# Performance work log

Measured on AMD Instinct MI355X. Metric: run time of the kernel, lower is better.

The kernel has to match this reference:

```python
import jax, jax.numpy as jnp
import numpy as np

N_NODES = 50000
N_EDGES = 800000
HIDDEN = 128
NUM_GDL = 2


def setup_inputs() -> dict:
    key = jax.random.key(0)
    k0, k1, k2, k3, k4 = jax.random.split(key, 5)
    x = jax.random.normal(k0, (N_NODES, HIDDEN), dtype=jnp.float32)
    row = jax.random.randint(k1, (N_EDGES,), 0, N_NODES, dtype=jnp.int32)
    # ensure every node appears at least once as a target so degree >= 1
    col_tail = jax.random.randint(k2, (N_EDGES - N_NODES,), 0, N_NODES, dtype=jnp.int32)
    col = jnp.concatenate([jnp.arange(N_NODES, dtype=jnp.int32), col_tail])
    edge_index = jnp.stack([row, col], axis=0)  # [2, E]
    W1s = jax.random.normal(k3, (NUM_GDL, HIDDEN, HIDDEN), dtype=jnp.float32) / np.sqrt(HIDDEN).astype(np.float32)
    W2s = jax.random.normal(k4, (NUM_GDL, HIDDEN, 2 * HIDDEN), dtype=jnp.float32) / np.sqrt(2 * HIDDEN).astype(np.float32)
    biases = jnp.zeros((NUM_GDL, HIDDEN), dtype=jnp.float32)  # reset_parameters zeroes bias
    return {"x": x, "edge_index": edge_index, "W1s": W1s, "W2s": W2s, "biases": biases}


def reference(x, edge_index, W1s, W2s, biases):
    # eval mode: dropout is identity
    row, col = edge_index[0], edge_index[1]  # row = source j, col = target i
    n, d = x.shape
    deg = jax.ops.segment_sum(jnp.ones(row.shape[0], x.dtype), col, num_segments=n)
    norm = (1.0 / deg)[row]  # per-edge norm, indexed by row as in torch source
    for k in range(W1s.shape[0]):
        W1, W2, b = W1s[k], W2s[k], biases[k]
        # lin2(cat[x_i, x_j]) = x_i @ W2[:, :d].T + x_j @ W2[:, d:].T
        # precompute both node-level projections, then gather per edge (cheaper than per-edge GEMM)
        proj_i = x @ W2[:, :d].T  # [n, d]
        proj_j = x @ W2[:, d:].T  # [n, d]
        msg = norm[:, None] * (proj_i[col] + proj_j[row])  # [E, d]
        agg = jax.ops.segment_sum(msg, col, num_segments=n)  # scatter-add into targets
        out = x @ W1.T - agg + b
        x = jax.nn.gelu(out, approximate=False)  # torch nn.GELU default = exact erf
    return x
```

## Files before the change

### kernel.cpp

```cpp
#include <hip/hip_runtime.h>

#define N_NODES 50000
#define N_EDGES 800000
#define D 128
#define NBUCKET 196
#define CAP 8192
#define EPT 16
#define SCAT_BLOCKS 196
#define WCONV_BLOCKS 96
#define GEMM_TILES 391

typedef unsigned short ushort_t;
typedef __bf16 bf16x8 __attribute__((ext_vector_type(8)));
typedef float f32x4 __attribute__((ext_vector_type(4)));
typedef float f32x2 __attribute__((ext_vector_type(2)));

__device__ __forceinline__ ushort_t f2bf(float f) {
    unsigned u = __builtin_bit_cast(unsigned, f);
    u += 0x7FFFu + ((u >> 16) & 1u);
    return (ushort_t)(u >> 16);
}
__device__ __forceinline__ float bf2f(unsigned h16) {
    return __builtin_bit_cast(float, h16 << 16);
}

__global__ __launch_bounds__(256) void k_pre(const int* __restrict__ row, const int* __restrict__ col,
                                             int* __restrict__ bucket_cursor, unsigned* __restrict__ temp,
                                             const float* __restrict__ W1s, const float* __restrict__ W2s,
                                             ushort_t* __restrict__ Wb) {
    __shared__ int hist[NBUCKET];
    int b = blockIdx.x;
    if (b < SCAT_BLOCKS) {
        for (int t = threadIdx.x; t < NBUCKET; t += 256) hist[t] = 0;
        __syncthreads();
        int base = (b * 256 + threadIdx.x) * EPT;
        bool act = base < N_EDGES;
        int4 c[4], r[4];
        if (act) {
            #pragma unroll
            for (int q = 0; q < 4; ++q) c[q] = *(const int4*)(col + base + q * 4);
            #pragma unroll
            for (int q = 0; q < 4; ++q) r[q] = *(const int4*)(row + base + q * 4);
            #pragma unroll
            for (int q = 0; q < 4; ++q) {
                atomicAdd(&hist[c[q].x >> 8], 1); atomicAdd(&hist[c[q].y >> 8], 1);
                atomicAdd(&hist[c[q].z >> 8], 1); atomicAdd(&hist[c[q].w >> 8], 1);
            }
        }
        __syncthreads();
        for (int t = threadIdx.x; t < NBUCKET; t += 256) {
            int cnt = hist[t];
            hist[t] = cnt ? atomicAdd(&bucket_cursor[t], cnt) : 0;
        }
        __syncthreads();
        if (act) {
            #pragma unroll
            for (int q = 0; q < 4; ++q) {
                int cc[4] = { c[q].x, c[q].y, c[q].z, c[q].w };
                int rr[4] = { r[q].x, r[q].y, r[q].z, r[q].w };
                #pragma unroll
                for (int e = 0; e < 4; ++e) {
                    int bk = cc[e] >> 8;
                    int pos = atomicAdd(&hist[bk], 1);
                    temp[bk * CAP + pos] = (unsigned)rr[e] | ((unsigned)(cc[e] & 255) << 16);
                }
            }
        }
    } else {
        int c = (b - SCAT_BLOCKS) * 256 + threadIdx.x;
        int k = c / 12288, rem = c % 12288;
        int mat = rem / 4096, rr = (rem % 4096) / 32, col4 = rem % 32;
        const float* src = (mat == 0)
            ? (W1s + k * 16384 + rr * 128 + col4 * 4)
            : (W2s + k * 32768 + rr * 256 + (mat == 2 ? 128 : 0) + col4 * 4);
        float4 v = *(const float4*)src;
        ushort_t tmp[4] = { f2bf(v.x), f2bf(v.y), f2bf(v.z), f2bf(v.w) };
        *(uint2*)(Wb + ((size_t)(k * 3 + mat)) * 16384 + rr * 128 + col4 * 4) = *(const uint2*)tmp;
    }
}

template<bool AF32>
__device__ __forceinline__ void gemm_tile3(int m0,
                                           ushort_t (*As)[136], ushort_t (*Bs)[136],
                                           const void* __restrict__ xsrc,
                                           const ushort_t* __restrict__ Wl,
                                           const float* __restrict__ scl,
                                           ushort_t* __restrict__ Plb,
                                           ushort_t* __restrict__ Pi_,
                                           unsigned char* __restrict__ Pj8) {
    const int tid = threadIdx.x;
    if constexpr (AF32) {
        const float* xf = (const float*)xsrc;
        #pragma unroll
        for (int it = 0; it < 8; ++it) {
            int c = tid + it * 256;
            int r = c >> 4, kc = c & 15;
            uint4 v = make_uint4(0, 0, 0, 0);
            int gm = m0 + r;
            if (gm < N_NODES) {
                float4 p0 = *(const float4*)(xf + (size_t)gm * D + kc * 8);
                float4 p1 = *(const float4*)(xf + (size_t)gm * D + kc * 8 + 4);
                ushort_t __attribute__((aligned(16))) tmp[8] =
                    { f2bf(p0.x), f2bf(p0.y), f2bf(p0.z), f2bf(p0.w),
                      f2bf(p1.x), f2bf(p1.y), f2bf(p1.z), f2bf(p1.w) };
                v = *(const uint4*)tmp;
            }
            *(uint4*)&As[r][kc * 8] = v;
        }
    } else {
        const ushort_t* xb = (const ushort_t*)xsrc;
        #pragma unroll
        for (int it = 0; it < 8; ++it) {
            int c = tid + it * 256;
            int r = c >> 4, kc = c & 15;
            uint4 v = make_uint4(0, 0, 0, 0);
            int gm = m0 + r;
            if (gm < N_NODES) v = *(const uint4*)(xb + (size_t)gm * D + kc * 8);
            *(uint4*)&As[r][kc * 8] = v;
        }
    }
    const int w = tid >> 6, lane = tid & 63, quad = lane >> 4, r16 = lane & 15;
    const int arow0 = w * 32 + r16, arow1 = arow0 + 16;
    #pragma unroll
    for (int y = 0; y < 3; ++y) {
        const ushort_t* Wmat = Wl + (size_t)y * 16384;
        #pragma unroll
        for (int it = 0; it < 8; ++it) {
            int c = tid + it * 256;
            int r = c >> 4, kc = c & 15;
            *(uint4*)&Bs[r][kc * 8] = *(const uint4*)(Wmat + r * 128 + kc * 8);
        }
        __syncthreads();
        f32x4 acc[2][8];
        #pragma unroll
        for (int mt = 0; mt < 2; ++mt)
            #pragma unroll
            for (int nt = 0; nt < 8; ++nt) acc[mt][nt] = (f32x4){0.f, 0.f, 0.f, 0.f};
        #pragma unroll
        for (int k0 = 0; k0 < 128; k0 += 32) {
            bf16x8 a0 = __builtin_bit_cast(bf16x8, *(const uint4*)&As[arow0][k0 + quad * 8]);
            bf16x8 a1 = __builtin_bit_cast(bf16x8, *(const uint4*)&As[arow1][k0 + quad * 8]);
            #pragma unroll
            for (int nt = 0; nt < 8; ++nt) {
                bf16x8 b = __builtin_bit_cast(bf16x8, *(const uint4*)&Bs[nt * 16 + r16][k0 + quad * 8]);
                acc[0][nt] = __builtin_amdgcn_mfma_f32_16x16x32_bf16(b, a0, acc[0][nt], 0, 0, 0);
                acc[1][nt] = __builtin_amdgcn_mfma_f32_16x16x32_bf16(b, a1, acc[1][nt], 0, 0, 0);
            }
        }
        #pragma unroll
        for (int mt = 0; mt < 2; ++mt) {
            int gm = m0 + w * 32 + mt * 16 + r16;
            if (gm >= N_NODES) continue;
            if (y < 2) {
                ushort_t* Outp = (y == 0) ? Plb : Pi_;
                #pragma unroll
                for (int nt = 0; nt < 8; ++nt) {
                    ushort_t tmp[4] = { f2bf(acc[mt][nt][0]), f2bf(acc[mt][nt][1]),
                                        f2bf(acc[mt][nt][2]), f2bf(acc[mt][nt][3]) };
                    *(uint2*)(Outp + (size_t)gm * D + nt * 16 + quad * 4) = *(const uint2*)tmp;
                }
            } else {
                float sc = scl ? scl[gm] : 1.0f;
                #pragma unroll
                for (int nt = 0; nt < 8; ++nt) {
                    int v = __builtin_amdgcn_cvt_pk_fp8_f32(acc[mt][nt][0] * sc, acc[mt][nt][1] * sc, 0, false);
                    v = __builtin_amdgcn_cvt_pk_fp8_f32(acc[mt][nt][2] * sc, acc[mt][nt][3] * sc, v, true);
                    *(unsigned*)(Pj8 + (size_t)gm * D + nt * 16 + quad * 4) = (unsigned)v;
                }
            }
        }
        if (y < 2) __syncthreads();
    }
}

__global__ __launch_bounds__(256) void k_bsort_gemm(const unsigned* __restrict__ temp,
                                                    const int* __restrict__ bucket_cursor,
                                                    ushort_t* __restrict__ csr, int* __restrict__ off,
                                                    int* __restrict__ deg, float* __restrict__ inv_deg,
                                                    const float* __restrict__ xf,
                                                    const ushort_t* __restrict__ Wb,
                                                    ushort_t* __restrict__ Plb,
                                                    ushort_t* __restrict__ Pi_,
                                                    unsigned char* __restrict__ Pj8) {
    __shared__ __align__(16) ushort_t As[128][136];
    __shared__ __align__(16) ushort_t Bs[128][136];
    __shared__ int hist[256];
    __shared__ int sm[256];
    if (blockIdx.x < NBUCKET) {
        int b = blockIdx.x, t = threadIdx.x;
        int cnt = bucket_cursor[b];
        sm[t] = (t < b) ? bucket_cursor[t] : 0;
        __syncthreads();
        for (int o = 1; o < 256; o <<= 1) {
            int add = (t >= o) ? sm[t - o] : 0;
            __syncthreads();
            sm[t] += add;
            __syncthreads();
        }
        int gbase = sm[255];
        int tbase = b * CAP;
        hist[t] = 0;
        __syncthreads();
        int i = t;
        for (; i + 768 < cnt; i += 1024) {
            unsigned e0 = temp[tbase + i], e1 = temp[tbase + i + 256];
            unsigned e2 = temp[tbase + i + 512], e3 = temp[tbase + i + 768];
            atomicAdd(&hist[e0 >> 16], 1); atomicAdd(&hist[e1 >> 16], 1);
            atomicAdd(&hist[e2 >> 16], 1); atomicAdd(&hist[e3 >> 16], 1);
        }
        for (; i < cnt; i += 256) atomicAdd(&hist[temp[tbase + i] >> 16], 1);
        __syncthreads();
        int c = hist[t];
        sm[t] = c;
        __syncthreads();
        for (int o = 1; o < 256; o <<= 1) {
            int add = (t >= o) ? sm[t - o] : 0;
            __syncthreads();
            sm[t] += add;
            __syncthreads();
        }
        int excl = sm[t] - c;
        int node = b * 256 + t;
        if (node < N_NODES) {
            off[node] = gbase + excl;
            deg[node] = c;
            inv_deg[node] = 1.0f / (float)c;
        }
        __syncthreads();
        hist[t] = gbase + excl;
        __syncthreads();
        i = t;
        for (; i + 768 < cnt; i += 1024) {
            unsigned e0 = temp[tbase + i], e1 = temp[tbase + i + 256];
            unsigned e2 = temp[tbase + i + 512], e3 = temp[tbase + i + 768];
            int p0 = atomicAdd(&hist[e0 >> 16], 1);
            int p1 = atomicAdd(&hist[e1 >> 16], 1);
            int p2 = atomicAdd(&hist[e2 >> 16], 1);
            int p3 = atomicAdd(&hist[e3 >> 16], 1);
            csr[p0] = (ushort_t)e0; csr[p1] = (ushort_t)e1;
            csr[p2] = (ushort_t)e2; csr[p3] = (ushort_t)e3;
        }
        for (; i < cnt; i += 256) {
            unsigned e = temp[tbase + i];
            int p = atomicAdd(&hist[e >> 16], 1);
            csr[p] = (ushort_t)e;
        }
    } else {
        gemm_tile3<true>((blockIdx.x - NBUCKET) * 128, As, Bs, xf, Wb, nullptr, Plb, Pi_, Pj8);
    }
}

__global__ __launch_bounds__(256) void k_gemm(const ushort_t* __restrict__ xb,
                                              const ushort_t* __restrict__ Wl,
                                              const float* __restrict__ inv_deg,
                                              ushort_t* __restrict__ Plb,
                                              ushort_t* __restrict__ Pi_,
                                              unsigned char* __restrict__ Pj8) {
    __shared__ __align__(16) ushort_t As[128][136];
    __shared__ __align__(16) ushort_t Bs[128][136];
    gemm_tile3<false>(blockIdx.x * 128, As, Bs, xb, Wl, inv_deg, Plb, Pi_, Pj8);
}

__global__ __launch_bounds__(256) void k_agg(const ushort_t* __restrict__ Plb,
                                             const ushort_t* __restrict__ Pi_,
                                             const unsigned char* __restrict__ Pj8,
                                             const int* __restrict__ off,
                                             const int* __restrict__ deg,
                                             const ushort_t* __restrict__ csr,
                                             const float* __restrict__ inv_deg,
                                             const float* __restrict__ bias,
                                             float* __restrict__ s_arr,
                                             float* __restrict__ out_f32,
                                             ushort_t* __restrict__ out_bf16,
                                             int layer0) {
    int wv = __builtin_amdgcn_readfirstlane(threadIdx.x >> 6);
    int node = blockIdx.x * 4 + wv;
    if (node >= N_NODES) return;
    const int lane = threadIdx.x & 63;
    const int g = lane >> 4;
    const int q8 = lane & 15;
    const int eoff = 8 * q8 + 2 * g;
    unsigned ulin = *(const unsigned*)(Plb + (size_t)node * D + eoff);
    unsigned upi  = *(const unsigned*)(Pi_ + (size_t)node * D + eoff);
    float2 bv = *(const float2*)(bias + eoff);
    float su[8];
    #pragma unroll
    for (int k = 0; k < 8; ++k) su[k] = 0.f;
    float sd = 0.f;
    const int e0 = off[node], ne = deg[node];
    int j = 0;
    if (layer0) {
        for (; j + 16 <= ne; j += 16) {
            int sx[4];
            #pragma unroll
            for (int t = 0; t < 4; ++t) sx[t] = csr[e0 + j + 4 * t + g];
            uint2 u[4];
            #pragma unroll
            for (int t = 0; t < 4; ++t) u[t] = *(const uint2*)(Pj8 + (size_t)sx[t] * D + 8 * q8);
            float dv[4];
            #pragma unroll
            for (int t = 0; t < 4; ++t) dv[t] = inv_deg[sx[t]];
            #pragma unroll
            for (int t = 0; t < 4; ++t) {
                f32x2 f0 = __builtin_amdgcn_cvt_pk_f32_fp8((int)u[t].x, false);
                f32x2 f1 = __builtin_amdgcn_cvt_pk_f32_fp8((int)u[t].x, true);
                f32x2 f2 = __builtin_amdgcn_cvt_pk_f32_fp8((int)u[t].y, false);
                f32x2 f3 = __builtin_amdgcn_cvt_pk_f32_fp8((int)u[t].y, true);
                sd += dv[t];
                su[0] += dv[t] * f0[0]; su[1] += dv[t] * f0[1];
                su[2] += dv[t] * f1[0]; su[3] += dv[t] * f1[1];
                su[4] += dv[t] * f2[0]; su[5] += dv[t] * f2[1];
                su[6] += dv[t] * f3[0]; su[7] += dv[t] * f3[1];
            }
        }
        for (; j + 4 <= ne; j += 4) {
            int sx = csr[e0 + j + g];
            uint2 u = *(const uint2*)(Pj8 + (size_t)sx * D + 8 * q8);
            float dv = inv_deg[sx];
            f32x2 f0 = __builtin_amdgcn_cvt_pk_f32_fp8((int)u.x, false);
            f32x2 f1 = __builtin_amdgcn_cvt_pk_f32_fp8((int)u.x, true);
            f32x2 f2 = __builtin_amdgcn_cvt_pk_f32_fp8((int)u.y, false);
            f32x2 f3 = __builtin_amdgcn_cvt_pk_f32_fp8((int)u.y, true);
            sd += dv;
            su[0] += dv * f0[0]; su[1] += dv * f0[1];
            su[2] += dv * f1[0]; su[3] += dv * f1[1];
            su[4] += dv * f2[0]; su[5] += dv * f2[1];
            su[6] += dv * f3[0]; su[7] += dv * f3[1];
        }
        if (j < ne) {
            int r = ne - j;
            int gi = (g < r) ? g : (r - 1);
            int sx = csr[e0 + j + gi];
            uint2 u = *(const uint2*)(Pj8 + (size_t)sx * D + 8 * q8);
            float dv = (g < r) ? inv_deg[sx] : 0.f;
            f32x2 f0 = __builtin_amdgcn_cvt_pk_f32_fp8((int)u.x, false);
            f32x2 f1 = __builtin_amdgcn_cvt_pk_f32_fp8((int)u.x, true);
            f32x2 f2 = __builtin_amdgcn_cvt_pk_f32_fp8((int)u.y, false);
            f32x2 f3 = __builtin_amdgcn_cvt_pk_f32_fp8((int)u.y, true);
            sd += dv;
            su[0] += dv * f0[0]; su[1] += dv * f0[1];
            su[2] += dv * f1[0]; su[3] += dv * f1[1];
            su[4] += dv * f2[0]; su[5] += dv * f2[1];
            su[6] += dv * f3[0]; su[7] += dv * f3[1];
        }
    } else {
        for (; j + 16 <= ne; j += 16) {
            int sx[4];
            #pragma unroll
            for (int t = 0; t < 4; ++t) sx[t] = csr[e0 + j + 4 * t + g];
            uint2 u[4];
            #pragma unroll
            for (int t = 0; t < 4; ++t) u[t] = *(const uint2*)(Pj8 + (size_t)sx[t] * D + 8 * q8);
            #pragma unroll
            for (int t = 0; t < 4; ++t) {
                f32x2 f0 = __builtin_amdgcn_cvt_pk_f32_fp8((int)u[t].x, false);
                f32x2 f1 = __builtin_amdgcn_cvt_pk_f32_fp8((int)u[t].x, true);
                f32x2 f2 = __builtin_amdgcn_cvt_pk_f32_fp8((int)u[t].y, false);
                f32x2 f3 = __builtin_amdgcn_cvt_pk_f32_fp8((int)u[t].y, true);
                su[0] += f0[0]; su[1] += f0[1];
                su[2] += f1[0]; su[3] += f1[1];
                su[4] += f2[0]; su[5] += f2[1];
                su[6] += f3[0]; su[7] += f3[1];
            }
        }
        for (; j + 4 <= ne; j += 4) {
            int sx = csr[e0 + j + g];
            uint2 u = *(const uint2*)(Pj8 + (size_t)sx * D + 8 * q8);
            f32x2 f0 = __builtin_amdgcn_cvt_pk_f32_fp8((int)u.x, false);
            f32x2 f1 = __builtin_amdgcn_cvt_pk_f32_fp8((int)u.x, true);
            f32x2 f2 = __builtin_amdgcn_cvt_pk_f32_fp8((int)u.y, false);
            f32x2 f3 = __builtin_amdgcn_cvt_pk_f32_fp8((int)u.y, true);
            su[0] += f0[0]; su[1] += f0[1];
            su[2] += f1[0]; su[3] += f1[1];
            su[4] += f2[0]; su[5] += f2[1];
            su[6] += f3[0]; su[7] += f3[1];
        }
        if (j < ne) {
            int r = ne - j;
            int gi = (g < r) ? g : (r - 1);
            int sx = csr[e0 + j + gi];
            uint2 u = *(const uint2*)(Pj8 + (size_t)sx * D + 8 * q8);
            float wt = (g < r) ? 1.f : 0.f;
            f32x2 f0 = __builtin_amdgcn_cvt_pk_f32_fp8((int)u.x, false);
            f32x2 f1 = __builtin_amdgcn_cvt_pk_f32_fp8((int)u.x, true);
            f32x2 f2 = __builtin_amdgcn_cvt_pk_f32_fp8((int)u.y, false);
            f32x2 f3 = __builtin_amdgcn_cvt_pk_f32_fp8((int)u.y, true);
            su[0] += wt * f0[0]; su[1] += wt * f0[1];
            su[2] += wt * f1[0]; su[3] += wt * f1[1];
            su[4] += wt * f2[0]; su[5] += wt * f2[1];
            su[6] += wt * f3[0]; su[7] += wt * f3[1];
        }
    }
    #pragma unroll
    for (int k = 0; k < 8; ++k) {
        su[k] += __shfl_xor(su[k], 16);
        su[k] += __shfl_xor(su[k], 32);
    }
    float si;
    if (layer0) {
        sd += __shfl_xor(sd, 16);
        sd += __shfl_xor(sd, 32);
        si = sd;
        if (lane == 0) s_arr[node] = si;
    } else {
        si = s_arr[node];
    }
    float t0 = (g < 2) ? ((g == 0) ? su[0] : su[2]) : ((g == 2) ? su[4] : su[6]);
    float t1 = (g < 2) ? ((g == 0) ? su[1] : su[3]) : ((g == 2) ? su[5] : su[7]);
    float a0 = bf2f(ulin & 0xffffu) + bv.x - si * bf2f(upi & 0xffffu) - t0;
    float a1 = bf2f(ulin >> 16)     + bv.y - si * bf2f(upi >> 16)     - t1;
    float g0 = 0.5f * a0 * (1.0f + erff(a0 * 0.70710678118654752440f));
    float g1 = 0.5f * a1 * (1.0f + erff(a1 * 0.70710678118654752440f));
    if (layer0) {
        ushort_t tmp[2] = { f2bf(g0), f2bf(g1) };
        *(unsigned*)(out_bf16 + (size_t)node * D + eoff) = *(const unsigned*)tmp;
    } else {
        *(float2*)(out_f32 + (size_t)node * D + eoff) = make_float2(g0, g1);
    }
}

extern "C" void kernel_launch(void* const* d_in, const int* in_sizes, int n_in,
                              void* d_out, int out_size, void* d_ws, size_t ws_size,
                              hipStream_t stream) {
    const float* x      = (const float*)d_in[0];
    const int*   ei     = (const int*)d_in[1];
    const int*   rowp   = ei;
    const int*   colp   = ei + N_EDGES;
    const float* W1s    = (const float*)d_in[2];
    const float* W2s    = (const float*)d_in[3];
    const float* biases = (const float*)d_in[4];
    float* out = (float*)d_out;

    char* ws = (char*)d_ws;
    size_t o = 0;
    auto carve = [&](size_t bytes) -> void* {
        void* p = ws + o;
        o = (o + bytes + 255) & ~(size_t)255;
        return p;
    };
    int*           bucket_cursor = (int*)carve(NBUCKET * 4);
    int*           deg     = (int*)carve(N_NODES * 4);
    float*         inv_deg = (float*)carve(N_NODES * 4);
    int*           off     = (int*)carve(N_NODES * 4);
    float*         s_arr   = (float*)carve(N_NODES * 4);
    ushort_t*      csr     = (ushort_t*)carve((size_t)N_EDGES * 2);
    unsigned*      temp    = (unsigned*)carve((size_t)NBUCKET * CAP * 4);
    ushort_t*      xb      = (ushort_t*)carve((size_t)N_NODES * D * 2);
    ushort_t*      Wb      = (ushort_t*)carve((size_t)2 * 3 * 16384 * 2);
    ushort_t*      Plb     = (ushort_t*)carve((size_t)N_NODES * D * 2);
    ushort_t*      Pi_     = (ushort_t*)carve((size_t)N_NODES * D * 2);
    unsigned char* Pj8     = (unsigned char*)carve((size_t)N_NODES * D);
    if (o > ws_size) return;

    hipMemsetAsync(bucket_cursor, 0, NBUCKET * 4, stream);

    k_pre<<<SCAT_BLOCKS + WCONV_BLOCKS, 256, 0, stream>>>(rowp, colp, bucket_cursor, temp,
                                                          W1s, W2s, Wb);
    k_bsort_gemm<<<NBUCKET + GEMM_TILES, 256, 0, stream>>>(temp, bucket_cursor, csr, off,
                                                           deg, inv_deg, x, Wb, Plb, Pi_, Pj8);

    const int AB = (N_NODES + 3) / 4;
    k_agg<<<AB, 256, 0, stream>>>(Plb, Pi_, Pj8, off, deg, csr, inv_deg, biases, s_arr,
                                  nullptr, xb, 1);
    k_gemm<<<GEMM_TILES, 256, 0, stream>>>(xb, Wb + (size_t)3 * 16384, inv_deg, Plb, Pi_, Pj8);
    k_agg<<<AB, 256, 0, stream>>>(Plb, Pi_, Pj8, off, deg, csr, inv_deg, biases + 128, s_arr,
                                  out, nullptr, 0);
}
```

Baseline: 205.7 us.

## Fuse all stages into one persistent kernel with software grid barriers

After: 500.7 us. 2.43x slower.

```diff
diff --git a/kernel.cpp b/kernel.cpp
--- a/kernel.cpp
+++ b/kernel.cpp
@@ -6,9 +6,11 @@
 #define NBUCKET 196
 #define CAP 8192
 #define EPT 16
-#define SCAT_BLOCKS 196
-#define WCONV_BLOCKS 96
+#define SCAT_UNITS 196
+#define WCONV_UNITS 96
 #define GEMM_TILES 391
+#define AGG_UNITS 12500
+#define GRID 512
 
 typedef unsigned short ushort_t;
 typedef __bf16 bf16x8 __attribute__((ext_vector_type(8)));
@@ -24,58 +26,138 @@
     return __builtin_bit_cast(float, h16 << 16);
 }
 
-__global__ __launch_bounds__(256) void k_pre(const int* __restrict__ row, const int* __restrict__ col,
-                                             int* __restrict__ bucket_cursor, unsigned* __restrict__ temp,
-                                             const float* __restrict__ W1s, const float* __restrict__ W2s,
-                                             ushort_t* __restrict__ Wb) {
-    __shared__ int hist[NBUCKET];
-    int b = blockIdx.x;
-    if (b < SCAT_BLOCKS) {
-        for (int t = threadIdx.x; t < NBUCKET; t += 256) hist[t] = 0;
-        __syncthreads();
-        int base = (b * 256 + threadIdx.x) * EPT;
-        bool act = base < N_EDGES;
-        int4 c[4], r[4];
-        if (act) {
-            #pragma unroll
-            for (int q = 0; q < 4; ++q) c[q] = *(const int4*)(col + base + q * 4);
-            #pragma unroll
-            for (int q = 0; q < 4; ++q) r[q] = *(const int4*)(row + base + q * 4);
-            #pragma unroll
-            for (int q = 0; q < 4; ++q) {
-                atomicAdd(&hist[c[q].x >> 8], 1); atomicAdd(&hist[c[q].y >> 8], 1);
-                atomicAdd(&hist[c[q].z >> 8], 1); atomicAdd(&hist[c[q].w >> 8], 1);
-            }
-        }
-        __syncthreads();
-        for (int t = threadIdx.x; t < NBUCKET; t += 256) {
-            int cnt = hist[t];
-            hist[t] = cnt ? atomicAdd(&bucket_cursor[t], cnt) : 0;
-        }
-        __syncthreads();
-        if (act) {
-            #pragma unroll
-            for (int q = 0; q < 4; ++q) {
-                int cc[4] = { c[q].x, c[q].y, c[q].z, c[q].w };
-                int rr[4] = { r[q].x, r[q].y, r[q].z, r[q].w };
-                #pragma unroll
-                for (int e = 0; e < 4; ++e) {
-                    int bk = cc[e] >> 8;
-                    int pos = atomicAdd(&hist[bk], 1);
-                    temp[bk * CAP + pos] = (unsigned)rr[e] | ((unsigned)(cc[e] & 255) << 16);
-                }
-            }
-        }
-    } else {
-        int c = (b - SCAT_BLOCKS) * 256 + threadIdx.x;
-        int k = c / 12288, rem = c % 12288;
-        int mat = rem / 4096, rr = (rem % 4096) / 32, col4 = rem % 32;
-        const float* src = (mat == 0)
-            ? (W1s + k * 16384 + rr * 128 + col4 * 4)
-            : (W2s + k * 32768 + rr * 256 + (mat == 2 ? 128 : 0) + col4 * 4);
-        float4 v = *(const float4*)src;
-        ushort_t tmp[4] = { f2bf(v.x), f2bf(v.y), f2bf(v.z), f2bf(v.w) };
-        *(uint2*)(Wb + ((size_t)(k * 3 + mat)) * 16384 + rr * 128 + col4 * 4) = *(const uint2*)tmp;
+union __align__(16) LdsU {
+    struct { ushort_t As[128][136]; ushort_t Bs[128][136]; } g;
+    struct { int hist[256]; int sm[256]; } s;
+};
+
+__device__ __forceinline__ void gsync(int* bar, int target) {
+    __syncthreads();
+    if (threadIdx.x == 0) {
+        __threadfence();
+        __hip_atomic_fetch_add(bar, 1, __ATOMIC_RELAXED, __HIP_MEMORY_SCOPE_AGENT);
+        while (__hip_atomic_load(bar, __ATOMIC_RELAXED, __HIP_MEMORY_SCOPE_AGENT) < target)
+            __builtin_amdgcn_s_sleep(2);
+        __threadfence();
+    }
+    __syncthreads();
+}
+
+__device__ __forceinline__ void scatter_unit(int u, int* hist,
+                                             const int* __restrict__ row, const int* __restrict__ col,
+                                             int* __restrict__ bucket_cursor, unsigned* __restrict__ temp) {
+    for (int t = threadIdx.x; t < NBUCKET; t += 256) hist[t] = 0;
+    __syncthreads();
+    int base = (u * 256 + threadIdx.x) * EPT;
+    bool act = base < N_EDGES;
+    int4 c[4], r[4];
+    if (act) {
+        #pragma unroll
+        for (int q = 0; q < 4; ++q) c[q] = *(const int4*)(col + base + q * 4);
+        #pragma unroll
+        for (int q = 0; q < 4; ++q) r[q] = *(const int4*)(row + base + q * 4);
+        #pragma unroll
+        for (int q = 0; q < 4; ++q) {
+            atomicAdd(&hist[c[q].x >> 8], 1); atomicAdd(&hist[c[q].y >> 8], 1);
+            atomicAdd(&hist[c[q].z >> 8], 1); atomicAdd(&hist[c[q].w >> 8], 1);
+        }
+    }
+    __syncthreads();
+    for (int t = threadIdx.x; t < NBUCKET; t += 256) {
+        int cnt = hist[t];
+        hist[t] = cnt ? atomicAdd(&bucket_cursor[t], cnt) : 0;
+    }
+    __syncthreads();
+    if (act) {
+        #pragma unroll
+        for (int q = 0; q < 4; ++q) {
+            int cc[4] = { c[q].x, c[q].y, c[q].z, c[q].w };
+            int rr[4] = { r[q].x, r[q].y, r[q].z, r[q].w };
+            #pragma unroll
+            for (int e = 0; e < 4; ++e) {
+                int bk = cc[e] >> 8;
+                int pos = atomicAdd(&hist[bk], 1);
+                temp[bk * CAP + pos] = (unsigned)rr[e] | ((unsigned)(cc[e] & 255) << 16);
+            }
+        }
+    }
+}
+
+__device__ __forceinline__ void wconv_unit(int u, const float* __restrict__ W1s,
+                                           const float* __restrict__ W2s, ushort_t* __restrict__ Wb) {
+    int c = u * 256 + threadIdx.x;
+    int k = c / 12288, rem = c % 12288;
+    int mat = rem / 4096, rr = (rem % 4096) / 32, col4 = rem % 32;
+    const float* src = (mat == 0)
+        ? (W1s + k * 16384 + rr * 128 + col4 * 4)
+        : (W2s + k * 32768 + rr * 256 + (mat == 2 ? 128 : 0) + col4 * 4);
+    float4 v = *(const float4*)src;
+    ushort_t tmp[4] = { f2bf(v.x), f2bf(v.y), f2bf(v.z), f2bf(v.w) };
+    *(uint2*)(Wb + ((size_t)(k * 3 + mat)) * 16384 + rr * 128 + col4 * 4) = *(const uint2*)tmp;
+}
+
+__device__ __forceinline__ void sort_unit(int b, int* hist, int* sm,
+                                          const unsigned* __restrict__ temp,
+                                          const int* __restrict__ bucket_cursor,
+                                          ushort_t* __restrict__ csr, int* __restrict__ off,
+                                          int* __restrict__ deg, float* __restrict__ inv_deg) {
+    int t = threadIdx.x;
+    int cnt = bucket_cursor[b];
+    sm[t] = (t < b) ? bucket_cursor[t] : 0;
+    __syncthreads();
+    for (int o = 1; o < 256; o <<= 1) {
+        int add = (t >= o) ? sm[t - o] : 0;
+        __syncthreads();
+        sm[t] += add;
+        __syncthreads();
+    }
+    int gbase = sm[255];
+    int tbase = b * CAP;
+    hist[t] = 0;
+    __syncthreads();
+    int i = t;
+    for (; i + 768 < cnt; i += 1024) {
+        unsigned e0 = temp[tbase + i], e1 = temp[tbase + i + 256];
+        unsigned e2 = temp[tbase + i + 512], e3 = temp[tbase + i + 768];
+        atomicAdd(&hist[e0 >> 16], 1); atomicAdd(&hist[e1 >> 16], 1);
+        atomicAdd(&hist[e2 >> 16], 1); atomicAdd(&hist[e3 >> 16], 1);
+    }
+    for (; i < cnt; i += 256) atomicAdd(&hist[temp[tbase + i] >> 16], 1);
+    __syncthreads();
+    int c = hist[t];
+    sm[t] = c;
+    __syncthreads();
+    for (int o = 1; o < 256; o <<= 1) {
+        int add = (t >= o) ? sm[t - o] : 0;
+        __syncthreads();
+        sm[t] += add;
+        __syncthreads();
+    }
+    int excl = sm[t] - c;
+    int node = b * 256 + t;
+    if (node < N_NODES) {
+        off[node] = gbase + excl;
+        deg[node] = c;
+        inv_deg[node] = 1.0f / (float)c;
+    }
+    __syncthreads();
+    hist[t] = gbase + excl;
+    __syncthreads();
+    i = t;
+    for (; i + 768 < cnt; i += 1024) {
+        unsigned e0 = temp[tbase + i], e1 = temp[tbase + i + 256];
+        unsigned e2 = temp[tbase + i + 512], e3 = temp[tbase + i + 768];
+        int p0 = atomicAdd(&hist[e0 >> 16], 1);
+        int p1 = atomicAdd(&hist[e1 >> 16], 1);
+        int p2 = atomicAdd(&hist[e2 >> 16], 1);
+        int p3 = atomicAdd(&hist[e3 >> 16], 1);
+        csr[p0] = (ushort_t)e0; csr[p1] = (ushort_t)e1;
+        csr[p2] = (ushort_t)e2; csr[p3] = (ushort_t)e3;
+    }
+    for (; i < cnt; i += 256) {
+        unsigned e = temp[tbase + i];
+        int p = atomicAdd(&hist[e >> 16], 1);
+        csr[p] = (ushort_t)e;
     }
 }
 
@@ -173,109 +255,21 @@
     }
 }
 
-__global__ __launch_bounds__(256) void k_bsort_gemm(const unsigned* __restrict__ temp,
-                                                    const int* __restrict__ bucket_cursor,
-                                                    ushort_t* __restrict__ csr, int* __restrict__ off,
-                                                    int* __restrict__ deg, float* __restrict__ inv_deg,
-                                                    const float* __restrict__ xf,
-                                                    const ushort_t* __restrict__ Wb,
-                                                    ushort_t* __restrict__ Plb,
-                                                    ushort_t* __restrict__ Pi_,
-                                                    unsigned char* __restrict__ Pj8) {
-    __shared__ __align__(16) ushort_t As[128][136];
-    __shared__ __align__(16) ushort_t Bs[128][136];
-    __shared__ int hist[256];
-    __shared__ int sm[256];
-    if (blockIdx.x < NBUCKET) {
-        int b = blockIdx.x, t = threadIdx.x;
-        int cnt = bucket_cursor[b];
-        sm[t] = (t < b) ? bucket_cursor[t] : 0;
-        __syncthreads();
-        for (int o = 1; o < 256; o <<= 1) {
-            int add = (t >= o) ? sm[t - o] : 0;
-            __syncthreads();
-            sm[t] += add;
-            __syncthreads();
-        }
-        int gbase = sm[255];
-        int tbase = b * CAP;
-        hist[t] = 0;
-        __syncthreads();
-        int i = t;
-        for (; i + 768 < cnt; i += 1024) {
-            unsigned e0 = temp[tbase + i], e1 = temp[tbase + i + 256];
-            unsigned e2 = temp[tbase + i + 512], e3 = temp[tbase + i + 768];
-            atomicAdd(&hist[e0 >> 16], 1); atomicAdd(&hist[e1 >> 16], 1);
-            atomicAdd(&hist[e2 >> 16], 1); atomicAdd(&hist[e3 >> 16], 1);
-        }
-        for (; i < cnt; i += 256) atomicAdd(&hist[temp[tbase + i] >> 16], 1);
-        __syncthreads();
-        int c = hist[t];
-        sm[t] = c;
-        __syncthreads();
-        for (int o = 1; o < 256; o <<= 1) {
-            int add = (t >= o) ? sm[t - o] : 0;
-            __syncthreads();
-            sm[t] += add;
-            __syncthreads();
-        }
-        int excl = sm[t] - c;
-        int node = b * 256 + t;
-        if (node < N_NODES) {
-            off[node] = gbase + excl;
-            deg[node] = c;
-            inv_deg[node] = 1.0f / (float)c;
-        }
-        __syncthreads();
-        hist[t] = gbase + excl;
-        __syncthreads();
-        i = t;
-        for (; i + 768 < cnt; i += 1024) {
-            unsigned e0 = temp[tbase + i], e1 = temp[tbase + i + 256];
-            unsigned e2 = temp[tbase + i + 512], e3 = temp[tbase + i + 768];
-            int p0 = atomicAdd(&hist[e0 >> 16], 1);
-            int p1 = atomicAdd(&hist[e1 >> 16], 1);
-            int p2 = atomicAdd(&hist[e2 >> 16], 1);
-            int p3 = atomicAdd(&hist[e3 >> 16], 1);
-            csr[p0] = (ushort_t)e0; csr[p1] = (ushort_t)e1;
-            csr[p2] = (ushort_t)e2; csr[p3] = (ushort_t)e3;
-        }
-        for (; i < cnt; i += 256) {
-            unsigned e = temp[tbase + i];
-            int p = atomicAdd(&hist[e >> 16], 1);
-            csr[p] = (ushort_t)e;
-        }
-    } else {
-        gemm_tile3<true>((blockIdx.x - NBUCKET) * 128, As, Bs, xf, Wb, nullptr, Plb, Pi_, Pj8);
-    }
-}
-
-__global__ __launch_bounds__(256) void k_gemm(const ushort_t* __restrict__ xb,
-                                              const ushort_t* __restrict__ Wl,
-                                              const float* __restrict__ inv_deg,
-                                              ushort_t* __restrict__ Plb,
-                                              ushort_t* __restrict__ Pi_,
-                                              unsigned char* __restrict__ Pj8) {
-    __shared__ __align__(16) ushort_t As[128][136];
-    __shared__ __align__(16) ushort_t Bs[128][136];
-    gemm_tile3<false>(blockIdx.x * 128, As, Bs, xb, Wl, inv_deg, Plb, Pi_, Pj8);
-}
-
-__global__ __launch_bounds__(256) void k_agg(const ushort_t* __restrict__ Plb,
-                                             const ushort_t* __restrict__ Pi_,
-                                             const unsigned char* __restrict__ Pj8,
-                                             const int* __restrict__ off,
-                                             const int* __restrict__ deg,
-                                             const ushort_t* __restrict__ csr,
-                                             const float* __restrict__ inv_deg,
-                                             const float* __restrict__ bias,
-                                             float* __restrict__ s_arr,
-                                             float* __restrict__ out_f32,
-                                             ushort_t* __restrict__ out_bf16,
-                                             int layer0) {
+template<int LAYER0>
+__device__ __forceinline__ void agg_unit(int u,
+                                         const ushort_t* __restrict__ Plb,
+                                         const ushort_t* __restrict__ Pi_,
+                                         const unsigned char* __restrict__ Pj8,
+                                         const int* __restrict__ off,
+                                         const int* __restrict__ deg,
+                                         const ushort_t* __restrict__ csr,
+                                         const float* __restrict__ inv_deg,
+                                         const float* __restrict__ bias,
+                                         float* __restrict__ s_arr,
+                                         float* __restrict__ out_f32,
+                                         ushort_t* __restrict__ out_bf16) {
     int wv = __builtin_amdgcn_readfirstlane(threadIdx.x >> 6);
-    int node = blockIdx.x * 4 + wv;
-    if (node >= N_NODES) return;
+    int node = u * 4 + wv;
     const int lane = threadIdx.x & 63;
     const int g = lane >> 4;
     const int q8 = lane & 15;
@@ -289,23 +283,23 @@
     float sd = 0.f;
     const int e0 = off[node], ne = deg[node];
     int j = 0;
-    if (layer0) {
+    if (LAYER0) {
         for (; j + 16 <= ne; j += 16) {
             int sx[4];
             #pragma unroll
             for (int t = 0; t < 4; ++t) sx[t] = csr[e0 + j + 4 * t + g];
-            uint2 u[4];
-            #pragma unroll
-            for (int t = 0; t < 4; ++t) u[t] = *(const uint2*)(Pj8 + (size_t)sx[t] * D + 8 * q8);
+            uint2 uu[4];
+            #pragma unroll
+            for (int t = 0; t < 4; ++t) uu[t] = *(const uint2*)(Pj8 + (size_t)sx[t] * D + 8 * q8);
             float dv[4];
             #pragma unroll
             for (int t = 0; t < 4; ++t) dv[t] = inv_deg[sx[t]];
             #pragma unroll
             for (int t = 0; t < 4; ++t) {
-                f32x2 f0 = __builtin_amdgcn_cvt_pk_f32_fp8((int)u[t].x, false);
-                f32x2 f1 = __builtin_amdgcn_cvt_pk_f32_fp8((int)u[t].x, true);
-                f32x2 f2 = __builtin_amdgcn_cvt_pk_f32_fp8((int)u[t].y, false);
-                f32x2 f3 = __builtin_amdgcn_cvt_pk_f32_fp8((int)u[t].y, true);
+                f32x2 f0 = __builtin_amdgcn_cvt_pk_f32_fp8((int)uu[t].x, false);
+                f32x2 f1 = __builtin_amdgcn_cvt_pk_f32_fp8((int)uu[t].x, true);
+                f32x2 f2 = __builtin_amdgcn_cvt_pk_f32_fp8((int)uu[t].y, false);
+                f32x2 f3 = __builtin_amdgcn_cvt_pk_f32_fp8((int)uu[t].y, true);
                 sd += dv[t];
                 su[0] += dv[t] * f0[0]; su[1] += dv[t] * f0[1];
                 su[2] += dv[t] * f1[0]; su[3] += dv[t] * f1[1];
@@ -315,12 +309,12 @@
         }
         for (; j + 4 <= ne; j += 4) {
             int sx = csr[e0 + j + g];
-            uint2 u = *(const uint2*)(Pj8 + (size_t)sx * D + 8 * q8);
+            uint2 uu = *(const uint2*)(Pj8 + (size_t)sx * D + 8 * q8);
             float dv = inv_deg[sx];
-            f32x2 f0 = __builtin_amdgcn_cvt_pk_f32_fp8((int)u.x, false);
-            f32x2 f1 = __builtin_amdgcn_cvt_pk_f32_fp8((int)u.x, true);
-            f32x2 f2 = __builtin_amdgcn_cvt_pk_f32_fp8((int)u.y, false);
-            f32x2 f3 = __builtin_amdgcn_cvt_pk_f32_fp8((int)u.y, true);
+            f32x2 f0 = __builtin_amdgcn_cvt_pk_f32_fp8((int)uu.x, false);
+            f32x2 f1 = __builtin_amdgcn_cvt_pk_f32_fp8((int)uu.x, true);
+            f32x2 f2 = __builtin_amdgcn_cvt_pk_f32_fp8((int)uu.y, false);
+            f32x2 f3 = __builtin_amdgcn_cvt_pk_f32_fp8((int)uu.y, true);
             sd += dv;
             su[0] += dv * f0[0]; su[1] += dv * f0[1];
             su[2] += dv * f1[0]; su[3] += dv * f1[1];
@@ -331,12 +325,12 @@
             int r = ne - j;
             int gi = (g < r) ? g : (r - 1);
             int sx = csr[e0 + j + gi];
-            uint2 u = *(const uint2*)(Pj8 + (size_t)sx * D + 8 * q8);
+            uint2 uu = *(const uint2*)(Pj8 + (size_t)sx * D + 8 * q8);
             float dv = (g < r) ? inv_deg[sx] : 0.f;
-            f32x2 f0 = __builtin_amdgcn_cvt_pk_f32_fp8((int)u.x, false);
-            f32x2 f1 = __builtin_amdgcn_cvt_pk_f32_fp8((int)u.x, true);
-            f32x2 f2 = __builtin_amdgcn_cvt_pk_f32_fp8((int)u.y, false);
-            f32x2 f3 = __builtin_amdgcn_cvt_pk_f32_fp8((int)u.y, true);
+            f32x2 f0 = __builtin_amdgcn_cvt_pk_f32_fp8((int)uu.x, false);
+            f32x2 f1 = __builtin_amdgcn_cvt_pk_f32_fp8((int)uu.x, true);
+            f32x2 f2 = __builtin_amdgcn_cvt_pk_f32_fp8((int)uu.y, false);
+            f32x2 f3 = __builtin_amdgcn_cvt_pk_f32_fp8((int)uu.y, true);
             sd += dv;
             su[0] += dv * f0[0]; su[1] += dv * f0[1];
             su[2] += dv * f1[0]; su[3] += dv * f1[1];
@@ -348,15 +342,15 @@
             int sx[4];
             #pragma unroll
             for (int t = 0; t < 4; ++t) sx[t] = csr[e0 + j + 4 * t + g];
-            uint2 u[4];
-            #pragma unroll
-            for (int t = 0; t < 4; ++t) u[t] = *(const uint2*)(Pj8 + (size_t)sx[t] * D + 8 * q8);
+            uint2 uu[4];
+            #pragma unroll
+            for (int t = 0; t < 4; ++t) uu[t] = *(const uint2*)(Pj8 + (size_t)sx[t] * D + 8 * q8);
             #pragma unroll
             for (int t = 0; t < 4; ++t) {
-                f32x2 f0 = __builtin_amdgcn_cvt_pk_f32_fp8((int)u[t].x, false);
-                f32x2 f1 = __builtin_amdgcn_cvt_pk_f32_fp8((int)u[t].x, true);
-                f32x2 f2 = __builtin_amdgcn_cvt_pk_f32_fp8((int)u[t].y, false);
-                f32x2 f3 = __builtin_amdgcn_cvt_pk_f32_fp8((int)u[t].y, true);
+                f32x2 f0 = __builtin_amdgcn_cvt_pk_f32_fp8((int)uu[t].x, false);
+                f32x2 f1 = __builtin_amdgcn_cvt_pk_f32_fp8((int)uu[t].x, true);
+                f32x2 f2 = __builtin_amdgcn_cvt_pk_f32_fp8((int)uu[t].y, false);
+                f32x2 f3 = __builtin_amdgcn_cvt_pk_f32_fp8((int)uu[t].y, true);
                 su[0] += f0[0]; su[1] += f0[1];
                 su[2] += f1[0]; su[3] += f1[1];
                 su[4] += f2[0]; su[5] += f2[1];
@@ -365,11 +359,11 @@
         }
         for (; j + 4 <= ne; j += 4) {
             int sx = csr[e0 + j + g];
-            uint2 u = *(const uint2*)(Pj8 + (size_t)sx * D + 8 * q8);
-            f32x2 f0 = __builtin_amdgcn_cvt_pk_f32_fp8((int)u.x, false);
-            f32x2 f1 = __builtin_amdgcn_cvt_pk_f32_fp8((int)u.x, true);
-            f32x2 f2 = __builtin_amdgcn_cvt_pk_f32_fp8((int)u.y, false);
-            f32x2 f3 = __builtin_amdgcn_cvt_pk_f32_fp8((int)u.y, true);
+            uint2 uu = *(const uint2*)(Pj8 + (size_t)sx * D + 8 * q8);
+            f32x2 f0 = __builtin_amdgcn_cvt_pk_f32_fp8((int)uu.x, false);
+            f32x2 f1 = __builtin_amdgcn_cvt_pk_f32_fp8((int)uu.x, true);
+            f32x2 f2 = __builtin_amdgcn_cvt_pk_f32_fp8((int)uu.y, false);
+            f32x2 f3 = __builtin_amdgcn_cvt_pk_f32_fp8((int)uu.y, true);
             su[0] += f0[0]; su[1] += f0[1];
             su[2] += f1[0]; su[3] += f1[1];
             su[4] += f2[0]; su[5] += f2[1];
@@ -379,12 +373,12 @@
             int r = ne - j;
             int gi = (g < r) ? g : (r - 1);
             int sx = csr[e0 + j + gi];
-            uint2 u = *(const uint2*)(Pj8 + (size_t)sx * D + 8 * q8);
+            uint2 uu = *(const uint2*)(Pj8 + (size_t)sx * D + 8 * q8);
             float wt = (g < r) ? 1.f : 0.f;
-            f32x2 f0 = __builtin_amdgcn_cvt_pk_f32_fp8((int)u.x, false);
-            f32x2 f1 = __builtin_amdgcn_cvt_pk_f32_fp8((int)u.x, true);
-            f32x2 f2 = __builtin_amdgcn_cvt_pk_f32_fp8((int)u.y, false);
-            f32x2 f3 = __builtin_amdgcn_cvt_pk_f32_fp8((int)u.y, true);
+            f32x2 f0 = __builtin_amdgcn_cvt_pk_f32_fp8((int)uu.x, false);
+            f32x2 f1 = __builtin_amdgcn_cvt_pk_f32_fp8((int)uu.x, true);
+            f32x2 f2 = __builtin_amdgcn_cvt_pk_f32_fp8((int)uu.y, false);
+            f32x2 f3 = __builtin_amdgcn_cvt_pk_f32_fp8((int)uu.y, true);
             su[0] += wt * f0[0]; su[1] += wt * f0[1];
             su[2] += wt * f1[0]; su[3] += wt * f1[1];
             su[4] += wt * f2[0]; su[5] += wt * f2[1];
@@ -397,7 +391,7 @@
         su[k] += __shfl_xor(su[k], 32);
     }
     float si;
-    if (layer0) {
+    if (LAYER0) {
         sd += __shfl_xor(sd, 16);
         sd += __shfl_xor(sd, 32);
         si = sd;
@@ -411,12 +405,54 @@
     float a1 = bf2f(ulin >> 16)     + bv.y - si * bf2f(upi >> 16)     - t1;
     float g0 = 0.5f * a0 * (1.0f + erff(a0 * 0.70710678118654752440f));
     float g1 = 0.5f * a1 * (1.0f + erff(a1 * 0.70710678118654752440f));
-    if (layer0) {
+    if (LAYER0) {
         ushort_t tmp[2] = { f2bf(g0), f2bf(g1) };
         *(unsigned*)(out_bf16 + (size_t)node * D + eoff) = *(const unsigned*)tmp;
     } else {
         *(float2*)(out_f32 + (size_t)node * D + eoff) = make_float2(g0, g1);
     }
+}
+
+__global__ __launch_bounds__(256, 2) void k_fused(
+        const float* __restrict__ x, const int* __restrict__ row, const int* __restrict__ col,
+        const float* __restrict__ W1s, const float* __restrict__ W2s,
+        const float* __restrict__ biases, float* __restrict__ out,
+        int* bar, int* bucket_cursor, unsigned* __restrict__ temp,
+        ushort_t* __restrict__ csr, int* __restrict__ off,
+        int* __restrict__ deg, float* __restrict__ inv_deg, float* __restrict__ s_arr,
+        ushort_t* __restrict__ xb, ushort_t* __restrict__ Wb,
+        ushort_t* __restrict__ Plb, ushort_t* __restrict__ Pi_,
+        unsigned char* __restrict__ Pj8) {
+    __shared__ LdsU lds;
+
+    for (int u = blockIdx.x; u < SCAT_UNITS + WCONV_UNITS; u += GRID) {
+        __syncthreads();
+        if (u < SCAT_UNITS) scatter_unit(u, lds.s.hist, row, col, bucket_cursor, temp);
+        else                wconv_unit(u - SCAT_UNITS, W1s, W2s, Wb);
+    }
+    gsync(bar, 1 * GRID);
+
+    for (int u = blockIdx.x; u < NBUCKET + GEMM_TILES; u += GRID) {
+        __syncthreads();
+        if (u < NBUCKET) sort_unit(u, lds.s.hist, lds.s.sm, temp, bucket_cursor, csr, off, deg, inv_deg);
+        else             gemm_tile3<true>((u - NBUCKET) * 128, lds.g.As, lds.g.Bs, x, Wb,
+                                          nullptr, Plb, Pi_, Pj8);
+    }
+    gsync(bar, 2 * GRID);
+
+    for (int u = blockIdx.x; u < AGG_UNITS; u += GRID)
+        agg_unit<1>(u, Plb, Pi_, Pj8, off, deg, csr, inv_deg, biases, s_arr, nullptr, xb);
+    gsync(bar, 3 * GRID);
+
+    for (int u = blockIdx.x; u < GEMM_TILES; u += GRID) {
+        __syncthreads();
+        gemm_tile3<false>(u * 128, lds.g.As, lds.g.Bs, xb, Wb + (size_t)3 * 16384,
+                          inv_deg, Plb, Pi_, Pj8);
+    }
+    gsync(bar, 4 * GRID);
+
+    for (int u = blockIdx.x; u < AGG_UNITS; u += GRID)
+        agg_unit<0>(u, Plb, Pi_, Pj8, off, deg, csr, inv_deg, biases + 128, s_arr, out, nullptr);
 }
 
 extern "C" void kernel_launch(void* const* d_in, const int* in_sizes, int n_in,
@@ -438,6 +474,7 @@
         o = (o + bytes + 255) & ~(size_t)255;
         return p;
     };
+    int*           bar           = (int*)carve(4);
     int*           bucket_cursor = (int*)carve(NBUCKET * 4);
     int*           deg     = (int*)carve(N_NODES * 4);
     float*         inv_deg = (float*)carve(N_NODES * 4);
@@ -452,17 +489,9 @@
     unsigned char* Pj8     = (unsigned char*)carve((size_t)N_NODES * D);
     if (o > ws_size) return;
 
-    hipMemsetAsync(bucket_cursor, 0, NBUCKET * 4, stream);
-
-    k_pre<<<SCAT_BLOCKS + WCONV_BLOCKS, 256, 0, stream>>>(rowp, colp, bucket_cursor, temp,
-                                                          W1s, W2s, Wb);
-    k_bsort_gemm<<<NBUCKET + GEMM_TILES, 256, 0, stream>>>(temp, bucket_cursor, csr, off,
-                                                           deg, inv_deg, x, Wb, Plb, Pi_, Pj8);
-
-    const int AB = (N_NODES + 3) / 4;
-    k_agg<<<AB, 256, 0, stream>>>(Plb, Pi_, Pj8, off, deg, csr, inv_deg, biases, s_arr,
-                                  nullptr, xb, 1);
-    k_gemm<<<GEMM_TILES, 256, 0, stream>>>(xb, Wb + (size_t)3 * 16384, inv_deg, Plb, Pi_, Pj8);
-    k_agg<<<AB, 256, 0, stream>>>(Plb, Pi_, Pj8, off, deg, csr, inv_deg, biases + 128, s_arr,
-                                  out, nullptr, 0);
-}
+    hipMemsetAsync(ws, 0, 256 + NBUCKET * 4, stream);
+
+    k_fused<<<GRID, 256, 0, stream>>>(x, rowp, colp, W1s, W2s, biases, out,
+                                      bar, bucket_cursor, temp, csr, off, deg, inv_deg,
+                                      s_arr, xb, Wb, Plb, Pi_, Pj8);
+}
```

## Read GEMM B operand from global, drop Bs LDS, union LDS and set occupancy bounds

Applied to the files above, without the earlier changes.

New measurement: 238.3 us. 15.9% more time.

```diff
diff --git a/kernel.cpp b/kernel.cpp
--- a/kernel.cpp
+++ b/kernel.cpp
@@ -80,8 +80,7 @@
 }
 
 template<bool AF32>
-__device__ __forceinline__ void gemm_tile3(int m0,
-                                           ushort_t (*As)[136], ushort_t (*Bs)[136],
+__device__ __forceinline__ void gemm_tile3(int m0, ushort_t (*As)[136],
                                            const void* __restrict__ xsrc,
                                            const ushort_t* __restrict__ Wl,
                                            const float* __restrict__ scl,
@@ -119,18 +118,12 @@
             *(uint4*)&As[r][kc * 8] = v;
         }
     }
+    __syncthreads();
     const int w = tid >> 6, lane = tid & 63, quad = lane >> 4, r16 = lane & 15;
     const int arow0 = w * 32 + r16, arow1 = arow0 + 16;
     #pragma unroll
     for (int y = 0; y < 3; ++y) {
         const ushort_t* Wmat = Wl + (size_t)y * 16384;
-        #pragma unroll
-        for (int it = 0; it < 8; ++it) {
-            int c = tid + it * 256;
-            int r = c >> 4, kc = c & 15;
-            *(uint4*)&Bs[r][kc * 8] = *(const uint4*)(Wmat + r * 128 + kc * 8);
-        }
-        __syncthreads();
         f32x4 acc[2][8];
         #pragma unroll
         for (int mt = 0; mt < 2; ++mt)
@@ -142,7 +135,8 @@
             bf16x8 a1 = __builtin_bit_cast(bf16x8, *(const uint4*)&As[arow1][k0 + quad * 8]);
             #pragma unroll
             for (int nt = 0; nt < 8; ++nt) {
-                bf16x8 b = __builtin_bit_cast(bf16x8, *(const uint4*)&Bs[nt * 16 + r16][k0 + quad * 8]);
+                bf16x8 b = __builtin_bit_cast(bf16x8,
+                    *(const uint4*)(Wmat + (nt * 16 + r16) * 128 + k0 + quad * 8));
                 acc[0][nt] = __builtin_amdgcn_mfma_f32_16x16x32_bf16(b, a0, acc[0][nt], 0, 0, 0);
                 acc[1][nt] = __builtin_amdgcn_mfma_f32_16x16x32_bf16(b, a1, acc[1][nt], 0, 0, 0);
             }
@@ -169,24 +163,27 @@
                 }
             }
         }
-        if (y < 2) __syncthreads();
-    }
-}
-
-__global__ __launch_bounds__(256) void k_bsort_gemm(const unsigned* __restrict__ temp,
-                                                    const int* __restrict__ bucket_cursor,
-                                                    ushort_t* __restrict__ csr, int* __restrict__ off,
-                                                    int* __restrict__ deg, float* __restrict__ inv_deg,
-                                                    const float* __restrict__ xf,
-                                                    const ushort_t* __restrict__ Wb,
-                                                    ushort_t* __restrict__ Plb,
-                                                    ushort_t* __restrict__ Pi_,
-                                                    unsigned char* __restrict__ Pj8) {
-    __shared__ __align__(16) ushort_t As[128][136];
-    __shared__ __align__(16) ushort_t Bs[128][136];
-    __shared__ int hist[256];
-    __shared__ int sm[256];
+    }
+}
+
+union __align__(16) LdsBG {
+    ushort_t As[128][136];
+    struct { int hist[256]; int sm[256]; } s;
+};
+
+__global__ __launch_bounds__(256, 4) void k_bsort_gemm(const unsigned* __restrict__ temp,
+                                                       const int* __restrict__ bucket_cursor,
+                                                       ushort_t* __restrict__ csr, int* __restrict__ off,
+                                                       int* __restrict__ deg, float* __restrict__ inv_deg,
+                                                       const float* __restrict__ xf,
+                                                       const ushort_t* __restrict__ Wb,
+                                                       ushort_t* __restrict__ Plb,
+                                                       ushort_t* __restrict__ Pi_,
+                                                       unsigned char* __restrict__ Pj8) {
+    __shared__ LdsBG lds;
     if (blockIdx.x < NBUCKET) {
+        int* hist = lds.s.hist;
+        int* sm = lds.s.sm;
         int b = blockIdx.x, t = threadIdx.x;
         int cnt = bucket_cursor[b];
         sm[t] = (t < b) ? bucket_cursor[t] : 0;
@@ -246,33 +243,32 @@
             csr[p] = (ushort_t)e;
         }
     } else {
-        gemm_tile3<true>((blockIdx.x - NBUCKET) * 128, As, Bs, xf, Wb, nullptr, Plb, Pi_, Pj8);
-    }
-}
-
-__global__ __launch_bounds__(256) void k_gemm(const ushort_t* __restrict__ xb,
-                                              const ushort_t* __restrict__ Wl,
-                                              const float* __restrict__ inv_deg,
-                                              ushort_t* __restrict__ Plb,
-                                              ushort_t* __restrict__ Pi_,
-                                              unsigned char* __restrict__ Pj8) {
+        gemm_tile3<true>((blockIdx.x - NBUCKET) * 128, lds.As, xf, Wb, nullptr, Plb, Pi_, Pj8);
+    }
+}
+
+__global__ __launch_bounds__(256, 4) void k_gemm(const ushort_t* __restrict__ xb,
+                                                 const ushort_t* __restrict__ Wl,
+                                                 const float* __restrict__ inv_deg,
+                                                 ushort_t* __restrict__ Plb,
+                                                 ushort_t* __restrict__ Pi_,
+                                                 unsigned char* __restrict__ Pj8) {
     __shared__ __align__(16) ushort_t As[128][136];
-    __shared__ __align__(16) ushort_t Bs[128][136];
-    gemm_tile3<false>(blockIdx.x * 128, As, Bs, xb, Wl, inv_deg, Plb, Pi_, Pj8);
-}
-
-__global__ __launch_bounds__(256) void k_agg(const ushort_t* __restrict__ Plb,
-                                             const ushort_t* __restrict__ Pi_,
-                                             const unsigned char* __restrict__ Pj8,
-                                             const int* __restrict__ off,
-                                             const int* __restrict__ deg,
-                                             const ushort_t* __restrict__ csr,
-                                             const float* __restrict__ inv_deg,
-                                             const float* __restrict__ bias,
-                                             float* __restrict__ s_arr,
-                                             float* __restrict__ out_f32,
-                                             ushort_t* __restrict__ out_bf16,
-                                             int layer0) {
+    gemm_tile3<false>(blockIdx.x * 128, As, xb, Wl, inv_deg, Plb, Pi_, Pj8);
+}
+
+__global__ __launch_bounds__(256, 8) void k_agg(const ushort_t* __restrict__ Plb,
+                                                const ushort_t* __restrict__ Pi_,
+                                                const unsigned char* __restrict__ Pj8,
+                                                const int* __restrict__ off,
+                                                const int* __restrict__ deg,
+                                                const ushort_t* __restrict__ csr,
+                                                const float* __restrict__ inv_deg,
+                                                const float* __restrict__ bias,
+                                                float* __restrict__ s_arr,
+                                                float* __restrict__ out_f32,
+                                                ushort_t* __restrict__ out_bf16,
+                                                int layer0) {
     int wv = __builtin_amdgcn_readfirstlane(threadIdx.x >> 6);
     int node = blockIdx.x * 4 + wv;
     if (node >= N_NODES) return;
@@ -294,18 +290,18 @@
             int sx[4];
             #pragma unroll
             for (int t = 0; t < 4; ++t) sx[t] = csr[e0 + j + 4 * t + g];
-            uint2 u[4];
-            #pragma unroll
-            for (int t = 0; t < 4; ++t) u[t] = *(const uint2*)(Pj8 + (size_t)sx[t] * D + 8 * q8);
+            uint2 uu[4];
+            #pragma unroll
+            for (int t = 0; t < 4; ++t) uu[t] = *(const uint2*)(Pj8 + (size_t)sx[t] * D + 8 * q8);
             float dv[4];
             #pragma unroll
             for (int t = 0; t < 4; ++t) dv[t] = inv_deg[sx[t]];
             #pragma unroll
             for (int t = 0; t < 4; ++t) {
-                f32x2 f0 = __builtin_amdgcn_cvt_pk_f32_fp8((int)u[t].x, false);
-                f32x2 f1 = __builtin_amdgcn_cvt_pk_f32_fp8((int)u[t].x, true);
-                f32x2 f2 = __builtin_amdgcn_cvt_pk_f32_fp8((int)u[t].y, false);
-                f32x2 f3 = __builtin_amdgcn_cvt_pk_f32_fp8((int)u[t].y, true);
+                f32x2 f0 = __builtin_amdgcn_cvt_pk_f32_fp8((int)uu[t].x, false);
+                f32x2 f1 = __builtin_amdgcn_cvt_pk_f32_fp8((int)uu[t].x, true);
+                f32x2 f2 = __builtin_amdgcn_cvt_pk_f32_fp8((int)uu[t].y, false);
+                f32x2 f3 = __builtin_amdgcn_cvt_pk_f32_fp8((int)uu[t].y, true);
                 sd += dv[t];
                 su[0] += dv[t] * f0[0]; su[1] += dv[t] * f0[1];
                 su[2] += dv[t] * f1[0]; su[3] += dv[t] * f1[1];
@@ -315,12 +311,12 @@
         }
         for (; j + 4 <= ne; j += 4) {
             int sx = csr[e0 + j + g];
-            uint2 u = *(const uint2*)(Pj8 + (size_t)sx * D + 8 * q8);
+            uint2 uu = *(const uint2*)(Pj8 + (size_t)sx * D + 8 * q8);
             float dv = inv_deg[sx];
-            f32x2 f0 = __builtin_amdgcn_cvt_pk_f32_fp8((int)u.x, false);
-            f32x2 f1 = __builtin_amdgcn_cvt_pk_f32_fp8((int)u.x, true);
-            f32x2 f2 = __builtin_amdgcn_cvt_pk_f32_fp8((int)u.y, false);
-            f32x2 f3 = __builtin_amdgcn_cvt_pk_f32_fp8((int)u.y, true);
+            f32x2 f0 = __builtin_amdgcn_cvt_pk_f32_fp8((int)uu.x, false);
+            f32x2 f1 = __builtin_amdgcn_cvt_pk_f32_fp8((int)uu.x, true);
+            f32x2 f2 = __builtin_amdgcn_cvt_pk_f32_fp8((int)uu.y, false);
+            f32x2 f3 = __builtin_amdgcn_cvt_pk_f32_fp8((int)uu.y, true);
             sd += dv;
             su[0] += dv * f0[0]; su[1] += dv * f0[1];
             su[2] += dv * f1[0]; su[3] += dv * f1[1];
@@ -331,12 +327,12 @@
             int r = ne - j;
             int gi = (g < r) ? g : (r - 1);
             int sx = csr[e0 + j + gi];
-            uint2 u = *(const uint2*)(Pj8 + (size_t)sx * D + 8 * q8);
+            uint2 uu = *(const uint2*)(Pj8 + (size_t)sx * D + 8 * q8);
             float dv = (g < r) ? inv_deg[sx] : 0.f;
-            f32x2 f0 = __builtin_amdgcn_cvt_pk_f32_fp8((int)u.x, false);
-            f32x2 f1 = __builtin_amdgcn_cvt_pk_f32_fp8((int)u.x, true);
-            f32x2 f2 = __builtin_amdgcn_cvt_pk_f32_fp8((int)u.y, false);
-            f32x2 f3 = __builtin_amdgcn_cvt_pk_f32_fp8((int)u.y, true);
+            f32x2 f0 = __builtin_amdgcn_cvt_pk_f32_fp8((int)uu.x, false);
+            f32x2 f1 = __builtin_amdgcn_cvt_pk_f32_fp8((int)uu.x, true);
+            f32x2 f2 = __builtin_amdgcn_cvt_pk_f32_fp8((int)uu.y, false);
+            f32x2 f3 = __builtin_amdgcn_cvt_pk_f32_fp8((int)uu.y, true);
             sd += dv;
             su[0] += dv * f0[0]; su[1] += dv * f0[1];
             su[2] += dv * f1[0]; su[3] += dv * f1[1];
@@ -348,15 +344,15 @@
             int sx[4];
             #pragma unroll
             for (int t = 0; t < 4; ++t) sx[t] = csr[e0 + j + 4 * t + g];
-            uint2 u[4];
-            #pragma unroll
-            for (int t = 0; t < 4; ++t) u[t] = *(const uint2*)(Pj8 + (size_t)sx[t] * D + 8 * q8);
+            uint2 uu[4];
+            #pragma unroll
+            for (int t = 0; t < 4; ++t) uu[t] = *(const uint2*)(Pj8 + (size_t)sx[t] * D + 8 * q8);
             #pragma unroll
             for (int t = 0; t < 4; ++t) {
-                f32x2 f0 = __builtin_amdgcn_cvt_pk_f32_fp8((int)u[t].x, false);
-                f32x2 f1 = __builtin_amdgcn_cvt_pk_f32_fp8((int)u[t].x, true);
-                f32x2 f2 = __builtin_amdgcn_cvt_pk_f32_fp8((int)u[t].y, false);
-                f32x2 f3 = __builtin_amdgcn_cvt_pk_f32_fp8((int)u[t].y, true);
+                f32x2 f0 = __builtin_amdgcn_cvt_pk_f32_fp8((int)uu[t].x, false);
+                f32x2 f1 = __builtin_amdgcn_cvt_pk_f32_fp8((int)uu[t].x, true);
+                f32x2 f2 = __builtin_amdgcn_cvt_pk_f32_fp8((int)uu[t].y, false);
+                f32x2 f3 = __builtin_amdgcn_cvt_pk_f32_fp8((int)uu[t].y, true);
                 su[0] += f0[0]; su[1] += f0[1];
                 su[2] += f1[0]; su[3] += f1[1];
                 su[4] += f2[0]; su[5] += f2[1];
@@ -365,11 +361,11 @@
         }
         for (; j + 4 <= ne; j += 4) {
             int sx = csr[e0 + j + g];
-            uint2 u = *(const uint2*)(Pj8 + (size_t)sx * D + 8 * q8);
-            f32x2 f0 = __builtin_amdgcn_cvt_pk_f32_fp8((int)u.x, false);
-            f32x2 f1 = __builtin_amdgcn_cvt_pk_f32_fp8((int)u.x, true);
-            f32x2 f2 = __builtin_amdgcn_cvt_pk_f32_fp8((int)u.y, false);
-            f32x2 f3 = __builtin_amdgcn_cvt_pk_f32_fp8((int)u.y, true);
+            uint2 uu = *(const uint2*)(Pj8 + (size_t)sx * D + 8 * q8);
+            f32x2 f0 = __builtin_amdgcn_cvt_pk_f32_fp8((int)uu.x, false);
+            f32x2 f1 = __builtin_amdgcn_cvt_pk_f32_fp8((int)uu.x, true);
+            f32x2 f2 = __builtin_amdgcn_cvt_pk_f32_fp8((int)uu.y, false);
+            f32x2 f3 = __builtin_amdgcn_cvt_pk_f32_fp8((int)uu.y, true);
             su[0] += f0[0]; su[1] += f0[1];
             su[2] += f1[0]; su[3] += f1[1];
             su[4] += f2[0]; su[5] += f2[1];
@@ -379,12 +375,12 @@
             int r = ne - j;
             int gi = (g < r) ? g : (r - 1);
             int sx = csr[e0 + j + gi];
-            uint2 u = *(const uint2*)(Pj8 + (size_t)sx * D + 8 * q8);
+            uint2 uu = *(const uint2*)(Pj8 + (size_t)sx * D + 8 * q8);
             float wt = (g < r) ? 1.f : 0.f;
-            f32x2 f0 = __builtin_amdgcn_cvt_pk_f32_fp8((int)u.x, false);
-            f32x2 f1 = __builtin_amdgcn_cvt_pk_f32_fp8((int)u.x, true);
-            f32x2 f2 = __builtin_amdgcn_cvt_pk_f32_fp8((int)u.y, false);
-            f32x2 f3 = __builtin_amdgcn_cvt_pk_f32_fp8((int)u.y, true);
+            f32x2 f0 = __builtin_amdgcn_cvt_pk_f32_fp8((int)uu.x, false);
+            f32x2 f1 = __builtin_amdgcn_cvt_pk_f32_fp8((int)uu.x, true);
+            f32x2 f2 = __builtin_amdgcn_cvt_pk_f32_fp8((int)uu.y, false);
+            f32x2 f3 = __builtin_amdgcn_cvt_pk_f32_fp8((int)uu.y, true);
             su[0] += wt * f0[0]; su[1] += wt * f0[1];
             su[2] += wt * f1[0]; su[3] += wt * f1[1];
             su[4] += wt * f2[0]; su[5] += wt * f2[1];
```
